# Kernel tuning notes

Measured on AMD Instinct MI355X. Metric: run time of the kernel, lower is better.

The kernel has to match this reference:

```python
import jax, jax.numpy as jnp
import numpy as np

N_ROWS = 100000   # sparse matrix rows (nodes)
N_COLS = 8192     # input feature dim
UNITS = 128
NNZ = 2000000     # ~20 nonzeros per row


def setup_inputs() -> dict:
    key = jax.random.key(0)
    k1, k2, k3, k4, k5 = jax.random.split(key, 5)
    vals = jax.random.normal(k1, (NNZ,), dtype=jnp.float32)
    rows = jax.random.randint(k2, (NNZ,), 0, N_ROWS, dtype=jnp.int32)
    cols = jax.random.randint(k3, (NNZ,), 0, N_COLS, dtype=jnp.int32)
    # GlorotUniform-style scale for W, matching the TF initializer statistics
    limit = jnp.sqrt(6.0 / (N_COLS + UNITS)).astype(jnp.float32)
    W = jax.random.uniform(k4, (N_COLS, UNITS), dtype=jnp.float32, minval=-limit, maxval=limit)
    b = jax.random.uniform(k5, (UNITS,), dtype=jnp.float32, minval=-limit, maxval=limit)
    return {"vals": vals, "rows": rows, "cols": cols, "W": W, "b": b, "num_rows": N_ROWS}


def reference(vals, rows, cols, W, b, num_rows):
    # sparse (COO) [num_rows, F] @ dense W [F, units]:
    # gather the W row for each nonzero, scale by the nonzero value,
    # then scatter-add into the output row -> segment_sum over `rows`.
    gathered = W[cols] * vals[:, None]            # [nnz, units]
    out = jax.ops.segment_sum(gathered, rows, num_segments=num_rows)  # [num_rows, units]
    return out + b                                 # bias add (use_bias=True)
```

## Files before the change

### kernel.cpp

```cpp
#include <hip/hip_runtime.h>
#include <hip/hip_fp16.h>


#define UNITS 128
#define SCAN_BLK 1024
#define BROW 98
#define NBC_PAD 1040
#define BCAP 2528
#define CH2 8192
#define SPILL_CAP 8192


__global__ __launch_bounds__(256) void setup_kernel(
        const float* __restrict__ W, __half2* __restrict__ Wh,
        int* __restrict__ ccur, int* __restrict__ spill_cnt,
        int nbc, int wn2 ) {
    int t = blockIdx.x * blockDim.x + threadIdx.x;
    if (t < nbc) ccur[t] = t * BCAP;
    if (t == nbc) *spill_cnt = 0;
    int stride = gridDim.x * blockDim.x;
    const float2* W2 = (const float2*)W;
    for (int i = t; i < wn2; i += stride)
        Wh[i] = __float22half2_rn(W2[i]);
}


__global__ __launch_bounds__(512, 6) void partition_kernel(
        const float* __restrict__ vals, const int* __restrict__ rows,
        const int* __restrict__ cols, int* __restrict__ ccur,
        float2* __restrict__ sortedA, int* __restrict__ spill_cnt,
        float2* __restrict__ spill, int nnz, int nbc) {
    __shared__ int hist[NBC_PAD];

    const int t = threadIdx.x;
    const int chunk0 = blockIdx.x * CH2;

    for (int s = t; s < NBC_PAD; s += 512) hist[s] = 0;
    __syncthreads();

    int rbuf[16];
#pragma unroll
    for (int j = 0; j < 16; ++j) {
        int i = chunk0 + j * 512 + t;
        int row = (i < nnz) ? rows[i] : -1;
        rbuf[j] = row;
        if (row >= 0) atomicAdd(&hist[row / BROW], 1);
    }
    __syncthreads();

    for (int s = t; s < nbc; s += 512) {
        int c = hist[s];
        int g = (c > 0) ? atomicAdd(&ccur[s], c) : 0;
        hist[s] = g;
    }
    __syncthreads();

#pragma unroll
    for (int j = 0; j < 16; ++j) {
        int row = rbuf[j];
        if (row < 0) continue;
        int i = chunk0 + j * 512 + t;
        int bkt = row / BROW;
        int rowlo = row - bkt * BROW;
        int dest = atomicAdd(&hist[bkt], 1);
        float v = vals[i];
        int col = cols[i];
        if (dest < (bkt + 1) * BCAP) {
            sortedA[dest] = make_float2(v, __int_as_float(col | (rowlo << 13)));
        } else {
            int sp = atomicAdd(spill_cnt, 1);
            if (sp < SPILL_CAP)
                spill[sp] = make_float2(v, __int_as_float(col | (row << 13)));
        }
    }
}


__global__ __launch_bounds__(512, 8) void fused_sort_compute_kernel(
        const float2* __restrict__ A, const int* __restrict__ ccur,
        const __half2* __restrict__ Wh, const float* __restrict__ b,
        float* __restrict__ out, const int* __restrict__ spill_cnt,
        const float2* __restrict__ spill, int NR) {
    __shared__ float2 st[BCAP + 8];
    __shared__ int cnt_s[128];
    __shared__ int rs[132];
    __shared__ int spill_n;
    const int t = threadIdx.x;
    const int lane = t & 63;
    const int w = t >> 6;
    const int bb = blockIdx.x;
    const int r0 = bb * BROW;
    const int gstart = bb * BCAP;
    int cnt = ccur[bb] - gstart;
    if (cnt > BCAP) cnt = BCAP;

    const float2 bias = ((const float2*)b)[lane];

    if (t < 128) cnt_s[t] = 0;
    if (t == 0) {
        int sn = *spill_cnt;
        spill_n = (sn > SPILL_CAP) ? SPILL_CAP : sn;
    }
    __syncthreads();

    float2 e[5];
#pragma unroll
    for (int j = 0; j < 5; ++j) {
        int k = j * 512 + t;
        if (k < cnt) {
            e[j] = A[gstart + k];
            atomicAdd(&cnt_s[(__float_as_int(e[j].y) >> 13) & 127], 1);
        }
    }
    __syncthreads();

    if (t < 128) rs[t] = cnt_s[t];
    __syncthreads();
    for (int off = 1; off < 128; off <<= 1) {
        int v = (t < 128 && t >= off) ? rs[t - off] : 0;
        __syncthreads();
        if (t < 128) rs[t] += v;
        __syncthreads();
    }
    int excl = (t < 128) ? rs[t] - cnt_s[t] : 0;
    __syncthreads();
    if (t < 128) { rs[t] = excl; cnt_s[t] = excl; }
    if (t == 0) rs[128] = cnt;
    __syncthreads();

#pragma unroll
    for (int j = 0; j < 5; ++j) {
        int k = j * 512 + t;
        if (k < cnt) {
            int pk = __float_as_int(e[j].y);
            int p = atomicAdd(&cnt_s[(pk >> 13) & 127], 1);
            st[p] = make_float2(e[j].x, __int_as_float(pk & 8191));
        }
    }
    __syncthreads();

    const int sn = spill_n;
    for (int r = w; r < BROW; r += 8) {
        int grow = r0 + r;
        if (grow >= NR) break;
        int s = rs[r], ee = rs[r + 1];
        float ax0 = 0.f, ay0 = 0.f, ax1 = 0.f, ay1 = 0.f;
        for (int k = s; k < ee; k += 4) {
            float2 p0 = st[k];
            float2 p1 = st[k + 1];
            float2 p2 = st[k + 2];
            float2 p3 = st[k + 3];
            int c0 = __float_as_int(p0.y) & 8191;
            int c1 = __float_as_int(p1.y) & 8191;
            int c2 = __float_as_int(p2.y) & 8191;
            int c3 = __float_as_int(p3.y) & 8191;
            float v0 = p0.x;
            float v1 = (k + 1 < ee) ? p1.x : 0.f;
            float v2 = (k + 2 < ee) ? p2.x : 0.f;
            float v3 = (k + 3 < ee) ? p3.x : 0.f;
            float2 w0 = __half22float2(Wh[c0 * 64 + lane]);
            float2 w1 = __half22float2(Wh[c1 * 64 + lane]);
            float2 w2 = __half22float2(Wh[c2 * 64 + lane]);
            float2 w3 = __half22float2(Wh[c3 * 64 + lane]);
            ax0 += v0 * w0.x; ay0 += v0 * w0.y;
            ax1 += v1 * w1.x; ay1 += v1 * w1.y;
            ax0 += v2 * w2.x; ay0 += v2 * w2.y;
            ax1 += v3 * w3.x; ay1 += v3 * w3.y;
        }
        for (int s2 = 0; s2 < sn; ++s2) {
            float2 es = spill[s2];
            int pk = __float_as_int(es.y);
            if ((pk >> 13) == grow) {
                float2 wv = __half22float2(Wh[(pk & 8191) * 64 + lane]);
                ax0 += es.x * wv.x; ay0 += es.x * wv.y;
            }
        }
        ((float2*)out)[(size_t)grow * 64 + lane] =
            make_float2(ax0 + ax1 + bias.x, ay0 + ay1 + bias.y);
    }
}


__global__ void hist_kernel(const int* __restrict__ rows, int* __restrict__ counts, int nnz) {
    int i = blockIdx.x * blockDim.x + threadIdx.x;
    if (i < nnz) atomicAdd(&counts[rows[i]], 1);
}

__global__ void scan1_kernel(const int* __restrict__ counts, int* __restrict__ tmp,
                             int* __restrict__ bsums, int NR, int NS) {
    __shared__ int s[SCAN_BLK];
    int t = threadIdx.x;
    int i = blockIdx.x * SCAN_BLK + t;
    int x = (i < NR) ? counts[i] : 0;
    s[t] = x;
    __syncthreads();
    for (int off = 1; off < SCAN_BLK; off <<= 1) {
        int v = (t >= off) ? s[t - off] : 0;
        __syncthreads();
        s[t] += v;
        __syncthreads();
    }
    if (i < NS) tmp[i] = s[t] - x;
    if (t == SCAN_BLK - 1) bsums[blockIdx.x] = s[SCAN_BLK - 1];
}

__global__ void scan2_kernel(int* __restrict__ bsums, int nb) {
    if (threadIdx.x == 0 && blockIdx.x == 0) {
        int run = 0;
        for (int i = 0; i < nb; ++i) { int c = bsums[i]; bsums[i] = run; run += c; }
    }
}

__global__ void scan3_kernel(const int* __restrict__ tmp, const int* __restrict__ bsums,
                             int* __restrict__ row_start, int* __restrict__ cursor,
                             int NR, int NS) {
    int i = blockIdx.x * blockDim.x + threadIdx.x;
    if (i < NS) {
        int v = tmp[i] + bsums[i >> 10];
        row_start[i] = v;
        if (i < NR) cursor[i] = v;
    }
}

__global__ void scatter_sort_kernel(const float* __restrict__ vals, const int* __restrict__ rows,
                                    const int* __restrict__ cols, int* __restrict__ cursor,
                                    float2* __restrict__ sorted, int nnz) {
    int i = blockIdx.x * blockDim.x + threadIdx.x;
    if (i < nnz) {
        int r = rows[i];
        int p = atomicAdd(&cursor[r], 1);
        sorted[p] = make_float2(vals[i], __int_as_float(cols[i]));
    }
}

__global__ void compute_kernel(const float2* __restrict__ sorted, const int* __restrict__ row_start,
                               const float* __restrict__ W, const float* __restrict__ b,
                               float* __restrict__ out, int NR) {
    int lane = threadIdx.x & 63;
    int wv = threadIdx.x >> 6;
    int row = blockIdx.x * 4 + wv;
    if (row >= NR) return;
    int start = row_start[row];
    int end   = row_start[row + 1];
    const float2* W2 = (const float2*)W;
    float accx0 = 0.f, accy0 = 0.f, accx1 = 0.f, accy1 = 0.f;
    for (int base = start; base < end; base += 64) {
        int m = end - base;
        if (m > 64) m = 64;
        float2 p = make_float2(0.f, __int_as_float(0));
        if (lane < m) p = sorted[base + lane];
        int vi = __float_as_int(p.x);
        int ci = __float_as_int(p.y);
        int rounds = (m + 3) & ~3;
        for (int j = 0; j < rounds; j += 4) {
            float v0 = __int_as_float(__builtin_amdgcn_readlane(vi, j));
            int   c0 = __builtin_amdgcn_readlane(ci, j);
            float v1 = __int_as_float(__builtin_amdgcn_readlane(vi, j + 1));
            int   c1 = __builtin_amdgcn_readlane(ci, j + 1);
            float v2 = __int_as_float(__builtin_amdgcn_readlane(vi, j + 2));
            int   c2 = __builtin_amdgcn_readlane(ci, j + 2);
            float v3 = __int_as_float(__builtin_amdgcn_readlane(vi, j + 3));
            int   c3 = __builtin_amdgcn_readlane(ci, j + 3);
            float2 w0 = W2[c0 * 64 + lane];
            float2 w1 = W2[c1 * 64 + lane];
            float2 w2 = W2[c2 * 64 + lane];
            float2 w3 = W2[c3 * 64 + lane];
            accx0 += v0 * w0.x; accy0 += v0 * w0.y;
            accx1 += v1 * w1.x; accy1 += v1 * w1.y;
            accx0 += v2 * w2.x; accy0 += v2 * w2.y;
            accx1 += v3 * w3.x; accy1 += v3 * w3.y;
        }
    }
    float2 bb = ((const float2*)b)[lane];
    ((float2*)out)[(size_t)row * 64 + lane] =
        make_float2(accx0 + accx1 + bb.x, accy0 + accy1 + bb.y);
}


__global__ void init_bias_kernel(float* __restrict__ out, const float* __restrict__ b, int total4) {
    const float4* b4 = (const float4*)b;
    float4* out4 = (float4*)out;
    int stride = gridDim.x * blockDim.x;
    for (int j = blockIdx.x * blockDim.x + threadIdx.x; j < total4; j += stride)
        out4[j] = b4[j & 31];
}

__global__ void scatter_atomic_kernel(const float* __restrict__ vals, const int* __restrict__ rows,
                                      const int* __restrict__ cols, const float* __restrict__ W,
                                      float* __restrict__ out, int nnz) {
    long long idx = (long long)blockIdx.x * blockDim.x + threadIdx.x;
    int i = (int)(idx >> 5);
    int c = (int)(idx & 31);
    if (i >= nnz) return;
    int row = rows[i], col = cols[i];
    float v = vals[i];
    float4 w = ((const float4*)W)[col * 32 + c];
    float* o = out + (size_t)row * UNITS + (c << 2);
    atomicAdd(o + 0, v * w.x);
    atomicAdd(o + 1, v * w.y);
    atomicAdd(o + 2, v * w.z);
    atomicAdd(o + 3, v * w.w);
}

extern "C" void kernel_launch(void* const* d_in, const int* in_sizes, int n_in,
                              void* d_out, int out_size, void* d_ws, size_t ws_size,
                              hipStream_t stream) {
    const float* vals = (const float*)d_in[0];
    const int*   rows = (const int*)d_in[1];
    const int*   cols = (const int*)d_in[2];
    const float* W    = (const float*)d_in[3];
    const float* b    = (const float*)d_in[4];
    float* out = (float*)d_out;

    const int nnz = in_sizes[0];
    const int NW  = in_sizes[3];
    const int NR  = out_size / UNITS;
    const int NS  = NR + 1;
    const int NB  = (NS + SCAN_BLK - 1) / SCAN_BLK;
    const int nbc = (NR + BROW - 1) / BROW;

    auto align = [](size_t x) { return (x + 255) & ~(size_t)255; };

    size_t off_ccur    = 0;
    size_t off_scnt    = align(off_ccur + (size_t)nbc * 4);
    size_t off_spill   = align(off_scnt + 4);
    size_t off_wh      = align(off_spill + (size_t)SPILL_CAP * 8);
    size_t off_sortedA = align(off_wh + (size_t)NW * 2);
    size_t needed_full = off_sortedA + (size_t)nbc * BCAP * 8;

    size_t t2_counts   = 0;
    size_t t2_tmp      = align(t2_counts + (size_t)NR * 4);
    size_t t2_bsums    = align(t2_tmp    + (size_t)NS * 4);
    size_t t2_rowstart = align(t2_bsums  + (size_t)NB * 4);
    size_t t2_cursor   = align(t2_rowstart + (size_t)NS * 4);
    size_t t2_sorted   = align(t2_cursor + (size_t)NR * 4);
    size_t needed_r2   = t2_sorted + (size_t)nnz * 8;

    char* ws = (char*)d_ws;

    if (ws_size >= needed_full && nbc <= NBC_PAD) {
        int*     ccur      = (int*)(ws + off_ccur);
        int*     spill_cnt = (int*)(ws + off_scnt);
        float2*  spill     = (float2*)(ws + off_spill);
        __half2* Wh        = (__half2*)(ws + off_wh);
        float2*  sortedA   = (float2*)(ws + off_sortedA);

        setup_kernel<<<512, 256, 0, stream>>>(W, Wh, ccur, spill_cnt, nbc, NW / 2);
        {
            int grid = (nnz + CH2 - 1) / CH2;
            partition_kernel<<<grid, 512, 0, stream>>>(vals, rows, cols, ccur, sortedA,
                                                       spill_cnt, spill, nnz, nbc);
        }
        fused_sort_compute_kernel<<<nbc, 512, 0, stream>>>(sortedA, ccur, Wh, b, out,
                                                           spill_cnt, spill, NR);
    } else if (ws_size >= needed_r2) {
        int*    counts    = (int*)(ws + t2_counts);
        int*    tmp       = (int*)(ws + t2_tmp);
        int*    bsums     = (int*)(ws + t2_bsums);
        int*    row_start = (int*)(ws + t2_rowstart);
        int*    cursor    = (int*)(ws + t2_cursor);
        float2* sorted    = (float2*)(ws + t2_sorted);

        hipMemsetAsync(counts, 0, (size_t)NR * 4, stream);
        {
            int block = 256, grid = (nnz + block - 1) / block;
            hist_kernel<<<grid, block, 0, stream>>>(rows, counts, nnz);
        }
        scan1_kernel<<<NB, SCAN_BLK, 0, stream>>>(counts, tmp, bsums, NR, NS);
        scan2_kernel<<<1, 64, 0, stream>>>(bsums, NB);
        {
            int block = 256, grid = (NS + block - 1) / block;
            scan3_kernel<<<grid, block, 0, stream>>>(tmp, bsums, row_start, cursor, NR, NS);
        }
        {
            int block = 256, grid = (nnz + block - 1) / block;
            scatter_sort_kernel<<<grid, block, 0, stream>>>(vals, rows, cols, cursor, sorted, nnz);
        }
        {
            int grid = (NR + 3) / 4;
            compute_kernel<<<grid, 256, 0, stream>>>(sorted, row_start, W, b, out, NR);
        }
    } else {
        int total4 = out_size / 4;
        int block = 256;
        int grid = (total4 + block - 1) / block;
        init_bias_kernel<<<grid, block, 0, stream>>>(out, b, total4);
        long long total_threads = (long long)nnz * 32;
        long long g2 = (total_threads + block - 1) / block;
        scatter_atomic_kernel<<<(int)g2, block, 0, stream>>>(vals, rows, cols, W, out, nnz);
    }
}
```

Measured before the change: 176.7 us.

## Sort partition chunk locally in shared memory before scattering to buckets

The partition kernel now builds a block-local counting sort. It scans the bucket histogram in shared memory, writes a permutation of element indices into a shared array, and then has consecutive threads write consecutive destination slots, so global stores to sortedA coalesce by bucket instead of scattering. This costs an extra scan with several barriers, a re-read of rows/vals/cols in permuted order, and more shared memory, while the occupancy hint rises from 6 to 8. NBC_PAD shrinks to 1024 to match two elements per thread, which assumes nbc is at most 1024.

```diff
diff --git a/kernel.cpp b/kernel.cpp
--- a/kernel.cpp
+++ b/kernel.cpp
@@ -5,7 +5,7 @@
 #define UNITS 128
 #define SCAN_BLK 1024
 #define BROW 98
-#define NBC_PAD 1040
+#define NBC_PAD 1024
 #define BCAP 2528
 #define CH2 8192
 #define SPILL_CAP 8192
@@ -25,46 +25,79 @@
 }
 
 
-__global__ __launch_bounds__(512, 6) void partition_kernel(
+__global__ __launch_bounds__(512, 8) void partition_kernel(
         const float* __restrict__ vals, const int* __restrict__ rows,
         const int* __restrict__ cols, int* __restrict__ ccur,
         float2* __restrict__ sortedA, int* __restrict__ spill_cnt,
         float2* __restrict__ spill, int nnz, int nbc) {
+    __shared__ unsigned short invs[CH2];
     __shared__ int hist[NBC_PAD];
+    __shared__ int pref[NBC_PAD];
+    __shared__ int gdelta[NBC_PAD];
 
     const int t = threadIdx.x;
     const int chunk0 = blockIdx.x * CH2;
-
-    for (int s = t; s < NBC_PAD; s += 512) hist[s] = 0;
-    __syncthreads();
-
-    int rbuf[16];
+    int n = nnz - chunk0;
+    if (n > CH2) n = CH2;
+
+    hist[t] = 0; hist[t + 512] = 0;
+    __syncthreads();
+
+    int bk[16];
 #pragma unroll
     for (int j = 0; j < 16; ++j) {
-        int i = chunk0 + j * 512 + t;
-        int row = (i < nnz) ? rows[i] : -1;
-        rbuf[j] = row;
-        if (row >= 0) atomicAdd(&hist[row / BROW], 1);
-    }
-    __syncthreads();
-
-    for (int s = t; s < nbc; s += 512) {
+        int r = j * 512 + t;
+        int bkt = -1;
+        if (r < n) {
+            bkt = rows[chunk0 + r] / BROW;
+            atomicAdd(&hist[bkt], 1);
+        }
+        bk[j] = bkt;
+    }
+    __syncthreads();
+
+    pref[t] = hist[t]; pref[t + 512] = hist[t + 512];
+    __syncthreads();
+    for (int off = 1; off < NBC_PAD; off <<= 1) {
+        int a0 = (t >= off) ? pref[t - off] : 0;
+        int a1 = (t + 512 >= off) ? pref[t + 512 - off] : 0;
+        __syncthreads();
+        pref[t] += a0; pref[t + 512] += a1;
+        __syncthreads();
+    }
+
+#pragma unroll
+    for (int u = 0; u < 2; ++u) {
+        int s = t + u * 512;
         int c = hist[s];
-        int g = (c > 0) ? atomicAdd(&ccur[s], c) : 0;
-        hist[s] = g;
+        int excl = pref[s] - c;
+        if (s < nbc) {
+            int g = (c > 0) ? atomicAdd(&ccur[s], c) : 0;
+            gdelta[s] = g - excl;
+        }
+        hist[s] = excl;
     }
     __syncthreads();
 
 #pragma unroll
     for (int j = 0; j < 16; ++j) {
-        int row = rbuf[j];
-        if (row < 0) continue;
-        int i = chunk0 + j * 512 + t;
+        int bkt = bk[j];
+        if (bkt >= 0) {
+            int pos = atomicAdd(&hist[bkt], 1);
+            invs[pos] = (unsigned short)(j * 512 + t);
+        }
+    }
+    __syncthreads();
+
+    for (int s = t; s < n; s += 512) {
+        int r = invs[s];
+        int i = chunk0 + r;
+        int row = rows[i];
+        float v = vals[i];
+        int col = cols[i];
         int bkt = row / BROW;
         int rowlo = row - bkt * BROW;
-        int dest = atomicAdd(&hist[bkt], 1);
-        float v = vals[i];
-        int col = cols[i];
+        int dest = gdelta[bkt] + s;
         if (dest < (bkt + 1) * BCAP) {
             sortedA[dest] = make_float2(v, __int_as_float(col | (rowlo << 13)));
         } else {
```

After: 169.6 us. 1.04x faster.
